# Optimization experiments

Hardware: AMD Instinct MI355X
Metric: run time of the kernel (lower is better)

The kernel has to match this reference:

```python
import jax, jax.numpy as jnp
import numpy as np

B, S, D, H = 2, 2048, 1024, 16
DK = D // H


def setup_inputs() -> dict:
    key = jax.random.key(0)
    ks = jax.random.split(key, 11)
    std = 1.0 / np.sqrt(D)
    inp = {
        "query": jax.random.normal(ks[0], (B, S, D), jnp.float32),
        "key": jax.random.normal(ks[1], (B, S, D), jnp.float32),
        "value": jax.random.normal(ks[2], (B, S, D), jnp.float32),
        # True = masked position (torch masked_fill semantics); causal mask
        "mask": jnp.triu(jnp.ones((1, 1, S, S), jnp.bool_), k=1),
        "Wq": jax.random.normal(ks[3], (D, D), jnp.float32) * std,
        "bq": jnp.zeros((D,), jnp.float32),
        "Wk": jax.random.normal(ks[4], (D, D), jnp.float32) * std,
        "bk": jnp.zeros((D,), jnp.float32),
        "Wv": jax.random.normal(ks[5], (D, D), jnp.float32) * std,
        "bv": jnp.zeros((D,), jnp.float32),
        "Wo": jax.random.normal(ks[6], (D, D), jnp.float32) * std,
        "bo": jnp.zeros((D,), jnp.float32),
    }
    return inp


def _split_heads(x):
    b, s, _ = x.shape
    return x.reshape(b, s, H, DK).transpose(0, 2, 1, 3)  # [b, H, s, dk]


def reference(query, key, value, mask, Wq, bq, Wk, bk, Wv, bv, Wo, bo):
    q = _split_heads(query @ Wq + bq)
    k = _split_heads(key @ Wk + bk)
    v = _split_heads(value @ Wv + bv)
    scale = 1.0 / (DK ** 0.5)
    logits = jnp.einsum("bhqd,bhkd->bhqk", q, k) * scale
    logits = jnp.where(mask, -1.0e9, logits)
    w = jax.nn.softmax(logits, axis=-1)
    att = jnp.einsum("bhqk,bhkd->bhqd", w, v)  # [B, H, S, dk]
    # NOTE: faithful to the original bug -- view() without permuting heads back,
    # i.e. a raw row-major reshape [B,H,S,dk] -> [B,S,H*dk].
    att = att.reshape(att.shape[0], att.shape[2], -1)
    out = att @ Wo + bo
    return out
```

## Files before the change

kernel.cpp:

```cpp
#include <hip/hip_runtime.h>
#include <hip/hip_bf16.h>

typedef __hip_bfloat16 bf16;
typedef __attribute__((ext_vector_type(8))) short bf16x8;
typedef __attribute__((ext_vector_type(4))) float f32x4;

constexpr int Bc  = 2;
constexpr int Sc  = 2048;
constexpr int Dc  = 1024;
constexpr int Hc  = 16;
constexpr int DKc = 64;

__device__ __forceinline__ float bfbits2f(unsigned short u) {
  return __uint_as_float(((unsigned)u) << 16);
}
__device__ __forceinline__ unsigned short f2bfbits(float x) {
  bf16 h = __float2bfloat16(x);
  return *reinterpret_cast<unsigned short*>(&h);
}
__device__ __forceinline__ void store1_dyn(char* base, size_t ei, int isf32, float v) {
  if (isf32) *reinterpret_cast<float*>(base + ei * 4) = v;
  else       *reinterpret_cast<bf16*>(base + ei * 2) = __float2bfloat16(v);
}
__device__ __forceinline__ float fast_exp2(float x) {
  return __builtin_amdgcn_exp2f(x);
}
__device__ __forceinline__ unsigned pkbf16(float a, float b) {
  __hip_bfloat162 h = __float22bfloat162_rn(make_float2(a, b));
  return *reinterpret_cast<unsigned*>(&h);
}
__device__ __forceinline__ uint4 pack8(const float4& a, const float4& b) {
  uint4 r;
  r.x = pkbf16(a.x, a.y);
  r.y = pkbf16(a.z, a.w);
  r.z = pkbf16(b.x, b.y);
  r.w = pkbf16(b.z, b.w);
  return r;
}
__device__ __forceinline__ void gld16(const void* g, void* l) {
  __builtin_amdgcn_global_load_lds(
      (const __attribute__((address_space(1))) unsigned int*)g,
      (__attribute__((address_space(3))) unsigned int*)l, 16, 0, 0);
}

__global__ void detect_dtype(const unsigned short* __restrict__ q, int* __restrict__ flag) {
  __shared__ int cnt[256];
  const int tid = threadIdx.x;
  int c = 0;
  for (int i = tid; i < 2048; i += 256) {
    const unsigned short u = q[i];
    const int e = (u >> 7) & 0xFF;
    if (e >= 134 || e <= 90) ++c;
  }
  cnt[tid] = c;
  __syncthreads();
  for (int s = 128; s > 0; s >>= 1) {
    if (tid < s) cnt[tid] += cnt[tid + s];
    __syncthreads();
  }
  if (tid == 0) flag[0] = (cnt[0] > 64) ? 1 : 0;
}

__global__ __launch_bounds__(256)
void prep_all(const char* __restrict__ W0, const char* __restrict__ W1,
              const char* __restrict__ W2, const char* __restrict__ W3,
              unsigned short* __restrict__ Wt_all,
              const char* __restrict__ b0, const char* __restrict__ b1,
              const char* __restrict__ b2, const char* __restrict__ b3,
              unsigned short* __restrict__ bb_all,
              const char* __restrict__ A0, const char* __restrict__ A1,
              const char* __restrict__ A2, bf16* __restrict__ B0,
              bf16* __restrict__ B1, bf16* __restrict__ B2,
              const int* __restrict__ flagp) {
  __shared__ unsigned short T[64][72];
  const int dyn = flagp[0];
  const int id = blockIdx.x;
  const int tid = threadIdx.x;

  if (id < 1024) {
    const int z = id >> 8, rem = id & 255;
    const int n0 = (rem & 15) * 64, k0 = (rem >> 4) * 64;
    const char* W = (z == 0) ? W0 : (z == 1) ? W1 : (z == 2) ? W2 : W3;
    unsigned short* Wt = Wt_all + (size_t)z * Dc * Dc;
    const int r = tid >> 2, c16 = (tid & 3) * 16;

    unsigned short us[16];
    if (dyn) {
      const float4* p = reinterpret_cast<const float4*>(
          W + ((size_t)(k0 + r) * Dc + n0 + c16) * 4);
      const float4 f0 = p[0], f1 = p[1], f2 = p[2], f3 = p[3];
      const float fv[16] = {f0.x, f0.y, f0.z, f0.w, f1.x, f1.y, f1.z, f1.w,
                            f2.x, f2.y, f2.z, f2.w, f3.x, f3.y, f3.z, f3.w};
#pragma unroll
      for (int i = 0; i < 16; ++i) us[i] = f2bfbits(fv[i]);
    } else {
      const ushort4* p = reinterpret_cast<const ushort4*>(
          W + ((size_t)(k0 + r) * Dc + n0 + c16) * 2);
      const ushort4 u0 = p[0], u1 = p[1], u2 = p[2], u3 = p[3];
      us[0] = u0.x;  us[1] = u0.y;  us[2] = u0.z;  us[3] = u0.w;
      us[4] = u1.x;  us[5] = u1.y;  us[6] = u1.z;  us[7] = u1.w;
      us[8] = u2.x;  us[9] = u2.y;  us[10] = u2.z; us[11] = u2.w;
      us[12] = u3.x; us[13] = u3.y; us[14] = u3.z; us[15] = u3.w;
    }
#pragma unroll
    for (int i = 0; i < 16; ++i) T[r][c16 + i] = us[i];
    __syncthreads();

    unsigned vs[8];
#pragma unroll
    for (int i = 0; i < 8; ++i)
      vs[i] = (unsigned)T[c16 + 2 * i][r] | ((unsigned)T[c16 + 2 * i + 1][r] << 16);
    uint4* op = reinterpret_cast<uint4*>(Wt + (size_t)(n0 + r) * Dc + k0 + c16);
    op[0] = make_uint4(vs[0], vs[1], vs[2], vs[3]);
    op[1] = make_uint4(vs[4], vs[5], vs[6], vs[7]);
  } else if (id < 2560) {
    const int j = id - 1024;
    const int z = j >> 9, x = j & 511;
    const char* src = (z == 0) ? A0 : (z == 1) ? A1 : A2;
    bf16* dst = (z == 0) ? B0 : (z == 1) ? B1 : B2;
    const size_t n = (size_t)4096 * Dc;
    const size_t stride = (size_t)512 * 256 * 8;
    for (size_t i = ((size_t)x * 256 + tid) * 8; i < n; i += stride) {
      uint4 u;
      if (dyn) {
        const float4* p = reinterpret_cast<const float4*>(src + i * 4);
        u = pack8(p[0], p[1]);
      } else {
        u = *reinterpret_cast<const uint4*>(src + i * 2);
      }
      *reinterpret_cast<uint4*>(dst + i) = u;
    }
  } else {
    const int x = id - 2560;
    const char* src = (x == 0) ? b0 : (x == 1) ? b1 : (x == 2) ? b2 : b3;
    for (int i = tid; i < Dc; i += 256) {
      float v = dyn ? reinterpret_cast<const float*>(src)[i]
                    : bfbits2f(reinterpret_cast<const unsigned short*>(src)[i]);
      bb_all[x * Dc + i] = f2bfbits(v);
    }
  }
}

__global__ __launch_bounds__(256)
void qkv_gemm_async(const bf16* __restrict__ A0, const bf16* __restrict__ A1,
                    const bf16* __restrict__ A2,
                    const unsigned short* __restrict__ Wt_all,
                    const unsigned short* __restrict__ bias_all,
                    bf16* __restrict__ C0, bf16* __restrict__ C1,
                    bf16* __restrict__ C2) {
  constexpr int K = Dc, N = Dc;
  __shared__ __align__(16) unsigned short At[128 * 32];
  __shared__ __align__(16) unsigned short Bt[128 * 32];

  const int z = blockIdx.z;
  const bf16* A = (z == 0) ? A0 : (z == 1) ? A1 : A2;
  bf16* C = (z == 0) ? C0 : (z == 1) ? C1 : C2;
  const float scale = (z == 0) ? 0.18033688011112042f : 1.0f;
  const unsigned short* Wt = Wt_all + (size_t)z * Dc * Dc;
  const unsigned short* bias = bias_all + z * Dc;

  const int tid = threadIdx.x;
  const int m0 = blockIdx.x * 128, n0 = blockIdx.y * 128;
  const int w = tid >> 6, lane = tid & 63;
  const int lo16 = lane & 15, quad = lane >> 4;
  const int wm = (w >> 1) * 64, wn = (w & 1) * 64;

  unsigned short* ldsA = &At[w * 1024 + lane * 8];
  unsigned short* ldsB = &Bt[w * 1024 + lane * 8];
  const bf16* gA = A + (size_t)(m0 + w * 32 + (lane >> 2)) * K + (lane & 3) * 8;
  const unsigned short* gB = Wt + (size_t)(n0 + w * 32 + (lane >> 2)) * K + (lane & 3) * 8;

  f32x4 acc[4][4] = {};

  for (int k0 = 0; k0 < K; k0 += 32) {
    gld16(gA + k0, ldsA);
    gld16(gA + (size_t)16 * K + k0, ldsA + 512);
    gld16(gB + k0, ldsB);
    gld16(gB + (size_t)16 * K + k0, ldsB + 512);
    __syncthreads();

    bf16x8 afr[4], bfr[4];
#pragma unroll
    for (int mt = 0; mt < 4; ++mt)
      afr[mt] = *reinterpret_cast<const bf16x8*>(&At[(wm + mt * 16 + lo16) * 32 + quad * 8]);
#pragma unroll
    for (int nt = 0; nt < 4; ++nt)
      bfr[nt] = *reinterpret_cast<const bf16x8*>(&Bt[(wn + nt * 16 + lo16) * 32 + quad * 8]);
#pragma unroll
    for (int mt = 0; mt < 4; ++mt)
#pragma unroll
      for (int nt = 0; nt < 4; ++nt)
        acc[mt][nt] = __builtin_amdgcn_mfma_f32_16x16x32_bf16(afr[mt], bfr[nt],
                                                              acc[mt][nt], 0, 0, 0);
    __syncthreads();
  }

  float bv[4];
#pragma unroll
  for (int nt = 0; nt < 4; ++nt)
    bv[nt] = bfbits2f(bias[n0 + wn + nt * 16 + lo16]);
#pragma unroll
  for (int mt = 0; mt < 4; ++mt)
#pragma unroll
    for (int r = 0; r < 4; ++r) {
      const int row = m0 + wm + mt * 16 + quad * 4 + r;
#pragma unroll
      for (int nt = 0; nt < 4; ++nt) {
        const int col = n0 + wn + nt * 16 + lo16;
        C[(size_t)row * N + col] = __float2bfloat16((acc[mt][nt][r] + bv[nt]) * scale);
      }
    }
}

__global__ __launch_bounds__(256)
void qkv_gemm(const char* __restrict__ A0, const char* __restrict__ A1,
              const char* __restrict__ A2, const unsigned short* __restrict__ Wt_all,
              const unsigned short* __restrict__ bias_all,
              bf16* __restrict__ C0, bf16* __restrict__ C1, bf16* __restrict__ C2,
              const int* __restrict__ flagp) {
  constexpr int K = Dc, N = Dc;
  __shared__ __align__(16) unsigned short At[128][32];
  __shared__ __align__(16) unsigned short Bt[128][32];

  const int z = blockIdx.z;
  const char* A = (z == 0) ? A0 : (z == 1) ? A1 : A2;
  bf16* C = (z == 0) ? C0 : (z == 1) ? C1 : C2;
  const float scale = (z == 0) ? 0.18033688011112042f : 1.0f;
  const unsigned short* Wt = Wt_all + (size_t)z * Dc * Dc;
  const unsigned short* bias = bias_all + z * Dc;
  const int af = flagp[0];

  const int tid = threadIdx.x;
  const int m0 = blockIdx.x * 128, n0 = blockIdx.y * 128;
  const int w = tid >> 6, lane = tid & 63;
  const int lo16 = lane & 15, quad = lane >> 4;
  const int wm = (w >> 1) * 64, wn = (w & 1) * 64;
  const int sr = tid >> 1, sh = (tid & 1) * 16;

  f32x4 acc[4][4] = {};

  for (int k0 = 0; k0 < K; k0 += 32) {
    uint4 a_lo, a_hi;
    if (af) {
      const float4* p = reinterpret_cast<const float4*>(
          A + ((size_t)(m0 + sr) * K + k0 + sh) * 4);
      a_lo = pack8(p[0], p[1]);
      a_hi = pack8(p[2], p[3]);
    } else {
      const uint4* p = reinterpret_cast<const uint4*>(
          A + ((size_t)(m0 + sr) * K + k0 + sh) * 2);
      a_lo = p[0];
      a_hi = p[1];
    }
    const uint4* wp = reinterpret_cast<const uint4*>(Wt + (size_t)(n0 + sr) * K + k0 + sh);
    const uint4 b_lo = wp[0], b_hi = wp[1];

    __syncthreads();
    *reinterpret_cast<uint4*>(&At[sr][sh])     = a_lo;
    *reinterpret_cast<uint4*>(&At[sr][sh + 8]) = a_hi;
    *reinterpret_cast<uint4*>(&Bt[sr][sh])     = b_lo;
    *reinterpret_cast<uint4*>(&Bt[sr][sh + 8]) = b_hi;
    __syncthreads();

    bf16x8 afr[4], bfr[4];
#pragma unroll
    for (int mt = 0; mt < 4; ++mt)
      afr[mt] = *reinterpret_cast<const bf16x8*>(&At[wm + mt * 16 + lo16][quad * 8]);
#pragma unroll
    for (int nt = 0; nt < 4; ++nt)
      bfr[nt] = *reinterpret_cast<const bf16x8*>(&Bt[wn + nt * 16 + lo16][quad * 8]);
#pragma unroll
    for (int mt = 0; mt < 4; ++mt)
#pragma unroll
      for (int nt = 0; nt < 4; ++nt)
        acc[mt][nt] = __builtin_amdgcn_mfma_f32_16x16x32_bf16(afr[mt], bfr[nt],
                                                              acc[mt][nt], 0, 0, 0);
  }

  float bv[4];
#pragma unroll
  for (int nt = 0; nt < 4; ++nt)
    bv[nt] = bfbits2f(bias[n0 + wn + nt * 16 + lo16]);
#pragma unroll
  for (int mt = 0; mt < 4; ++mt)
#pragma unroll
    for (int r = 0; r < 4; ++r) {
      const int row = m0 + wm + mt * 16 + quad * 4 + r;
#pragma unroll
      for (int nt = 0; nt < 4; ++nt) {
        const int col = n0 + wn + nt * 16 + lo16;
        C[(size_t)row * N + col] = __float2bfloat16((acc[mt][nt][r] + bv[nt]) * scale);
      }
    }
}

__global__ __launch_bounds__(256)
void out_gemm_async(const bf16* __restrict__ A, const unsigned short* __restrict__ Wt,
                    const unsigned short* __restrict__ bias, char* __restrict__ C,
                    const int* __restrict__ flagp) {
  constexpr int K = Dc, N = Dc;
  __shared__ __align__(16) unsigned short At[64 * 32];
  __shared__ __align__(16) unsigned short Bt[128 * 32];

  const int cf = flagp[0];
  const int tid = threadIdx.x;
  const int m0 = blockIdx.x * 64, n0 = blockIdx.y * 128;
  const int w = tid >> 6, lane = tid & 63;
  const int lo16 = lane & 15, quad = lane >> 4;
  const int wm = (w >> 1) * 32, wn = (w & 1) * 64;

  unsigned short* ldsA = &At[w * 512 + lane * 8];
  unsigned short* ldsB = &Bt[w * 1024 + lane * 8];
  const bf16* gA = A + (size_t)(m0 + w * 16 + (lane >> 2)) * K + (lane & 3) * 8;
  const unsigned short* gB = Wt + (size_t)(n0 + w * 32 + (lane >> 2)) * K + (lane & 3) * 8;

  f32x4 acc[2][4] = {};

  for (int k0 = 0; k0 < K; k0 += 32) {
    gld16(gA + k0, ldsA);
    gld16(gB + k0, ldsB);
    gld16(gB + (size_t)16 * K + k0, ldsB + 512);
    __syncthreads();

    bf16x8 afr[2], bfr[4];
#pragma unroll
    for (int mt = 0; mt < 2; ++mt)
      afr[mt] = *reinterpret_cast<const bf16x8*>(&At[(wm + mt * 16 + lo16) * 32 + quad * 8]);
#pragma unroll
    for (int nt = 0; nt < 4; ++nt)
      bfr[nt] = *reinterpret_cast<const bf16x8*>(&Bt[(wn + nt * 16 + lo16) * 32 + quad * 8]);
#pragma unroll
    for (int mt = 0; mt < 2; ++mt)
#pragma unroll
      for (int nt = 0; nt < 4; ++nt)
        acc[mt][nt] = __builtin_amdgcn_mfma_f32_16x16x32_bf16(afr[mt], bfr[nt],
                                                              acc[mt][nt], 0, 0, 0);
    __syncthreads();
  }

  float bv[4];
#pragma unroll
  for (int nt = 0; nt < 4; ++nt)
    bv[nt] = bfbits2f(bias[n0 + wn + nt * 16 + lo16]);
#pragma unroll
  for (int mt = 0; mt < 2; ++mt)
#pragma unroll
    for (int r = 0; r < 4; ++r) {
      const int row = m0 + wm + mt * 16 + quad * 4 + r;
#pragma unroll
      for (int nt = 0; nt < 4; ++nt) {
        const int col = n0 + wn + nt * 16 + lo16;
        store1_dyn(C, (size_t)row * N + col, cf, acc[mt][nt][r] + bv[nt]);
      }
    }
}

__global__ __launch_bounds__(512)
void attn_mfma(const bf16* __restrict__ Q, const bf16* __restrict__ K,
               const bf16* __restrict__ V, bf16* __restrict__ O) {
  __shared__ __align__(16) unsigned short Kt[64][72];
  __shared__ __align__(16) unsigned short Vt[64][72];
  __shared__ __align__(16) unsigned short St[8][16][72];
  __shared__ float Li[8][16];

  const int hb = blockIdx.x & 31;
  const int i  = blockIdx.x >> 5;
  const int g = i >> 3, r0 = i & 7;
  const int c = g ? (15 - r0) : r0;
  const int b = hb >> 4, h = hb & 15;
  const int q0 = c * 128;
  const int tid = threadIdx.x;
  const int w = tid >> 6;
  const int lane = tid & 63;
  const int lo16 = lane & 15, quad = lane >> 4;
  const size_t hd = (size_t)h * DKc;

  const int t256 = tid & 255;
  const int kr = t256 >> 2, kc = (t256 & 3) * 16;
  const int vk = (t256 & 31) * 2, vd0 = (t256 >> 5) * 8;
  const bool vrole = (w < 4);

  const bf16* qrow = Q + ((size_t)(b * Sc + q0 + w * 16 + lo16)) * Dc + hd;
  const bf16x8 qa0 = *reinterpret_cast<const bf16x8*>(qrow + quad * 8);
  const bf16x8 qa1 = *reinterpret_cast<const bf16x8*>(qrow + 32 + quad * 8);

  f32x4 oacc[4] = {f32x4{0,0,0,0}, f32x4{0,0,0,0}, f32x4{0,0,0,0}, f32x4{0,0,0,0}};
  float lsum = 0.f;
  const int qg  = q0 + w * 16 + lo16;
  const int qwm = q0 + w * 16 + 15;
  const int nt = 2 * (c + 1);

  const bf16* vsrc = V + ((size_t)(b * Sc + vk)) * Dc + hd + vd0;
  const bf16* ksrc = K + ((size_t)(b * Sc + kr)) * Dc + hd + kc;

  uint4 rA, rB;
  if (vrole) {
    rA = *reinterpret_cast<const uint4*>(vsrc);
    rB = *reinterpret_cast<const uint4*>(vsrc + Dc);
  } else {
    rA = *reinterpret_cast<const uint4*>(ksrc);
    rB = *reinterpret_cast<const uint4*>(ksrc + 8);
  }

  for (int t = 0; t < nt; ++t) {
    const int kt = t * 64;
    __syncthreads();
    if (vrole) {
      *reinterpret_cast<unsigned*>(&Vt[vd0 + 0][vk]) = (rA.x & 0xffffu) | (rB.x << 16);
      *reinterpret_cast<unsigned*>(&Vt[vd0 + 1][vk]) = (rA.x >> 16)     | (rB.x & 0xffff0000u);
      *reinterpret_cast<unsigned*>(&Vt[vd0 + 2][vk]) = (rA.y & 0xffffu) | (rB.y << 16);
      *reinterpret_cast<unsigned*>(&Vt[vd0 + 3][vk]) = (rA.y >> 16)     | (rB.y & 0xffff0000u);
      *reinterpret_cast<unsigned*>(&Vt[vd0 + 4][vk]) = (rA.z & 0xffffu) | (rB.z << 16);
      *reinterpret_cast<unsigned*>(&Vt[vd0 + 5][vk]) = (rA.z >> 16)     | (rB.z & 0xffff0000u);
      *reinterpret_cast<unsigned*>(&Vt[vd0 + 6][vk]) = (rA.w & 0xffffu) | (rB.w << 16);
      *reinterpret_cast<unsigned*>(&Vt[vd0 + 7][vk]) = (rA.w >> 16)     | (rB.w & 0xffff0000u);
    } else {
      *reinterpret_cast<uint4*>(&Kt[kr][kc])     = rA;
      *reinterpret_cast<uint4*>(&Kt[kr][kc + 8]) = rB;
    }
    __syncthreads();

    if (t + 1 < nt) {
      const size_t off = (size_t)(kt + 64) * Dc;
      if (vrole) {
        rA = *reinterpret_cast<const uint4*>(vsrc + off);
        rB = *reinterpret_cast<const uint4*>(vsrc + off + Dc);
      } else {
        rA = *reinterpret_cast<const uint4*>(ksrc + off);
        rB = *reinterpret_cast<const uint4*>(ksrc + off + 8);
      }
    }

    if (kt > qwm) continue;

    f32x4 s[4] = {f32x4{0,0,0,0}, f32x4{0,0,0,0}, f32x4{0,0,0,0}, f32x4{0,0,0,0}};
    __builtin_amdgcn_s_setprio(1);
#pragma unroll
    for (int ct = 0; ct < 4; ++ct) {
      const bf16x8 ka0 = *reinterpret_cast<const bf16x8*>(&Kt[ct * 16 + lo16][quad * 8]);
      const bf16x8 ka1 = *reinterpret_cast<const bf16x8*>(&Kt[ct * 16 + lo16][32 + quad * 8]);
      s[ct] = __builtin_amdgcn_mfma_f32_16x16x32_bf16(ka0, qa0, s[ct], 0, 0, 0);
      s[ct] = __builtin_amdgcn_mfma_f32_16x16x32_bf16(ka1, qa1, s[ct], 0, 0, 0);
    }
    __builtin_amdgcn_s_setprio(0);

    if (kt + 63 > q0 + w * 16) {
#pragma unroll
      for (int ct = 0; ct < 4; ++ct)
#pragma unroll
        for (int r = 0; r < 4; ++r)
          if (kt + ct * 16 + quad * 4 + r > qg) s[ct][r] = -1e9f;
    }

#pragma unroll
    for (int ct = 0; ct < 4; ++ct) {
      const float p0 = fast_exp2(s[ct][0]);
      const float p1 = fast_exp2(s[ct][1]);
      const float p2 = fast_exp2(s[ct][2]);
      const float p3 = fast_exp2(s[ct][3]);
      lsum += (p0 + p1) + (p2 + p3);
      uint2 pk;
      pk.x = pkbf16(p0, p1);
      pk.y = pkbf16(p2, p3);
      *reinterpret_cast<uint2*>(&St[w][lo16][ct * 16 + quad * 4]) = pk;
    }

    const bf16x8 pa0 = *reinterpret_cast<const bf16x8*>(&St[w][lo16][quad * 8]);
    const bf16x8 pa1 = *reinterpret_cast<const bf16x8*>(&St[w][lo16][32 + quad * 8]);
    __builtin_amdgcn_s_setprio(1);
#pragma unroll
    for (int ct = 0; ct < 4; ++ct) {
      const bf16x8 vb0 = *reinterpret_cast<const bf16x8*>(&Vt[ct * 16 + lo16][quad * 8]);
      const bf16x8 vb1 = *reinterpret_cast<const bf16x8*>(&Vt[ct * 16 + lo16][32 + quad * 8]);
      oacc[ct] = __builtin_amdgcn_mfma_f32_16x16x32_bf16(pa0, vb0, oacc[ct], 0, 0, 0);
      oacc[ct] = __builtin_amdgcn_mfma_f32_16x16x32_bf16(pa1, vb1, oacc[ct], 0, 0, 0);
    }
    __builtin_amdgcn_s_setprio(0);
  }

  lsum += __shfl_xor(lsum, 16);
  lsum += __shfl_xor(lsum, 32);
  if (quad == 0) Li[w][lo16] = 1.f / lsum;
  __builtin_amdgcn_wave_barrier();
  const f32x4 invv = *reinterpret_cast<const f32x4*>(&Li[w][quad * 4]);

#pragma unroll
  for (int r = 0; r < 4; ++r) {
    bf16* op = O + (((size_t)(b * Hc + h) * Sc) + q0 + w * 16 + quad * 4 + r) * DKc + lo16;
#pragma unroll
    for (int ct = 0; ct < 4; ++ct)
      op[ct * 16] = __float2bfloat16(oacc[ct][r] * invv[r]);
  }
}

extern "C" void kernel_launch(void* const* d_in, const int* in_sizes, int n_in,
                              void* d_out, int out_size, void* d_ws, size_t ws_size,
                              hipStream_t stream) {
  (void)in_sizes; (void)out_size;
  const char* query = (const char*)d_in[0];
  const char* key_  = (const char*)d_in[1];
  const char* value = (const char*)d_in[2];
  const int wb = n_in - 8;
  const char* Wq = (const char*)d_in[wb + 0];
  const char* bq = (const char*)d_in[wb + 1];
  const char* Wk = (const char*)d_in[wb + 2];
  const char* bk = (const char*)d_in[wb + 3];
  const char* Wv = (const char*)d_in[wb + 4];
  const char* bv = (const char*)d_in[wb + 5];
  const char* Wo = (const char*)d_in[wb + 6];
  const char* bo = (const char*)d_in[wb + 7];

  char* ws = (char*)d_ws;
  bf16* Qs  = (bf16*)(ws);
  bf16* Ks  = (bf16*)(ws + ((size_t)8  << 20));
  bf16* Vs  = (bf16*)(ws + ((size_t)16 << 20));
  bf16* att = (bf16*)(ws + ((size_t)24 << 20));
  unsigned short* Wt_all = (unsigned short*)(ws + ((size_t)32 << 20));
  unsigned short* bb_all = (unsigned short*)(ws + ((size_t)40 << 20));
  int* flag = (int*)(ws + ((size_t)40 << 20) + 16384);
  bf16* Qb = (bf16*)(ws + ((size_t)42 << 20));
  bf16* Kb = (bf16*)(ws + ((size_t)50 << 20));
  bf16* Vb = (bf16*)(ws + ((size_t)58 << 20));
  const bool big_ws = ws_size >= ((size_t)66 << 20);

  detect_dtype<<<1, 256, 0, stream>>>((const unsigned short*)query, flag);

  if (big_ws) {
    prep_all<<<2564, 256, 0, stream>>>(Wq, Wk, Wv, Wo, Wt_all, bq, bk, bv, bo,
                                       bb_all, query, key_, value, Qb, Kb, Vb, flag);
    qkv_gemm_async<<<dim3(32, 8, 3), 256, 0, stream>>>(Qb, Kb, Vb, Wt_all, bb_all,
                                                       Qs, Ks, Vs);
  } else {
    prep_all<<<1028, 256, 0, stream>>>(Wq, Wk, Wv, Wo, Wt_all, bq, bk, bv, bo,
                                       bb_all, query, key_, value,
                                       (bf16*)att, (bf16*)att, (bf16*)att, flag);
    qkv_gemm<<<dim3(32, 8, 3), 256, 0, stream>>>(query, key_, value, Wt_all, bb_all,
                                                 Qs, Ks, Vs, flag);
  }

  attn_mfma<<<dim3(512), 512, 0, stream>>>(Qs, Ks, Vs, att);

  out_gemm_async<<<dim3(64, 8), 256, 0, stream>>>(att, Wt_all + (size_t)3 * Dc * Dc,
                                                  bb_all + 3 * Dc, (char*)d_out, flag);
}
```

Measured before the change: 239.7 us.

## Load K fragments directly from global and double-buffer V tile with single barrier

The attention kernel stops staging K in shared memory. Each wave loads its K MFMA operands straight from global/L2 into registers. V staging is spread across all 512 threads with half-width loads, and the V tile is double-buffered so each iteration needs one barrier instead of two. Launch bounds now request higher occupancy. The trade-off is that each wave issues redundant global K reads (8 waves each read the full K tile) and pays more global latency on the critical path before the QK MFMAs.

```diff
diff --git a/kernel.cpp b/kernel.cpp
--- a/kernel.cpp
+++ b/kernel.cpp
@@ -355,11 +355,10 @@
     }
 }
 
-__global__ __launch_bounds__(512)
+__global__ __launch_bounds__(512, 4)
 void attn_mfma(const bf16* __restrict__ Q, const bf16* __restrict__ K,
                const bf16* __restrict__ V, bf16* __restrict__ O) {
-  __shared__ __align__(16) unsigned short Kt[64][72];
-  __shared__ __align__(16) unsigned short Vt[64][72];
+  __shared__ __align__(16) unsigned short Vt[2][64][72];
   __shared__ __align__(16) unsigned short St[8][16][72];
   __shared__ float Li[8][16];
 
@@ -375,10 +374,7 @@
   const int lo16 = lane & 15, quad = lane >> 4;
   const size_t hd = (size_t)h * DKc;
 
-  const int t256 = tid & 255;
-  const int kr = t256 >> 2, kc = (t256 & 3) * 16;
-  const int vk = (t256 & 31) * 2, vd0 = (t256 >> 5) * 8;
-  const bool vrole = (w < 4);
+  const int vk = (tid & 31) * 2, vd0 = (tid >> 5) * 4;
 
   const bf16* qrow = Q + ((size_t)(b * Sc + q0 + w * 16 + lo16)) * Dc + hd;
   const bf16x8 qa0 = *reinterpret_cast<const bf16x8*>(qrow + quad * 8);
@@ -390,92 +386,83 @@
   const int qwm = q0 + w * 16 + 15;
   const int nt = 2 * (c + 1);
 
-  const bf16* vsrc = V + ((size_t)(b * Sc + vk)) * Dc + hd + vd0;
-  const bf16* ksrc = K + ((size_t)(b * Sc + kr)) * Dc + hd + kc;
-
-  uint4 rA, rB;
-  if (vrole) {
-    rA = *reinterpret_cast<const uint4*>(vsrc);
-    rB = *reinterpret_cast<const uint4*>(vsrc + Dc);
-  } else {
-    rA = *reinterpret_cast<const uint4*>(ksrc);
-    rB = *reinterpret_cast<const uint4*>(ksrc + 8);
-  }
+  const bf16* vsrc  = V + ((size_t)(b * Sc + vk)) * Dc + hd + vd0;
+  const bf16* kfrag = K + ((size_t)(b * Sc) + lo16) * Dc + hd + quad * 8;
+
+  uint2 rA = *reinterpret_cast<const uint2*>(vsrc);
+  uint2 rB = *reinterpret_cast<const uint2*>(vsrc + Dc);
 
   for (int t = 0; t < nt; ++t) {
     const int kt = t * 64;
-    __syncthreads();
-    if (vrole) {
-      *reinterpret_cast<unsigned*>(&Vt[vd0 + 0][vk]) = (rA.x & 0xffffu) | (rB.x << 16);
-      *reinterpret_cast<unsigned*>(&Vt[vd0 + 1][vk]) = (rA.x >> 16)     | (rB.x & 0xffff0000u);
-      *reinterpret_cast<unsigned*>(&Vt[vd0 + 2][vk]) = (rA.y & 0xffffu) | (rB.y << 16);
-      *reinterpret_cast<unsigned*>(&Vt[vd0 + 3][vk]) = (rA.y >> 16)     | (rB.y & 0xffff0000u);
-      *reinterpret_cast<unsigned*>(&Vt[vd0 + 4][vk]) = (rA.z & 0xffffu) | (rB.z << 16);
-      *reinterpret_cast<unsigned*>(&Vt[vd0 + 5][vk]) = (rA.z >> 16)     | (rB.z & 0xffff0000u);
-      *reinterpret_cast<unsigned*>(&Vt[vd0 + 6][vk]) = (rA.w & 0xffffu) | (rB.w << 16);
-      *reinterpret_cast<unsigned*>(&Vt[vd0 + 7][vk]) = (rA.w >> 16)     | (rB.w & 0xffff0000u);
-    } else {
-      *reinterpret_cast<uint4*>(&Kt[kr][kc])     = rA;
-      *reinterpret_cast<uint4*>(&Kt[kr][kc + 8]) = rB;
-    }
-    __syncthreads();
+    const int p = t & 1;
+
+    *reinterpret_cast<unsigned*>(&Vt[p][vd0 + 0][vk]) = (rA.x & 0xffffu) | (rB.x << 16);
+    *reinterpret_cast<unsigned*>(&Vt[p][vd0 + 1][vk]) = (rA.x >> 16)     | (rB.x & 0xffff0000u);
+    *reinterpret_cast<unsigned*>(&Vt[p][vd0 + 2][vk]) = (rA.y & 0xffffu) | (rB.y << 16);
+    *reinterpret_cast<unsigned*>(&Vt[p][vd0 + 3][vk]) = (rA.y >> 16)     | (rB.y & 0xffff0000u);
+    __syncthreads();
+
+    const bool live = (kt <= qwm);
+
+    bf16x8 ka[4], kb[4];
+    if (live) {
+      const bf16* kp = kfrag + (size_t)kt * Dc;
+#pragma unroll
+      for (int ct = 0; ct < 4; ++ct) {
+        ka[ct] = *reinterpret_cast<const bf16x8*>(kp + (size_t)(ct * 16) * Dc);
+        kb[ct] = *reinterpret_cast<const bf16x8*>(kp + (size_t)(ct * 16) * Dc + 32);
+      }
+    }
 
     if (t + 1 < nt) {
-      const size_t off = (size_t)(kt + 64) * Dc;
-      if (vrole) {
-        rA = *reinterpret_cast<const uint4*>(vsrc + off);
-        rB = *reinterpret_cast<const uint4*>(vsrc + off + Dc);
-      } else {
-        rA = *reinterpret_cast<const uint4*>(ksrc + off);
-        rB = *reinterpret_cast<const uint4*>(ksrc + off + 8);
-      }
-    }
-
-    if (kt > qwm) continue;
-
-    f32x4 s[4] = {f32x4{0,0,0,0}, f32x4{0,0,0,0}, f32x4{0,0,0,0}, f32x4{0,0,0,0}};
-    __builtin_amdgcn_s_setprio(1);
-#pragma unroll
-    for (int ct = 0; ct < 4; ++ct) {
-      const bf16x8 ka0 = *reinterpret_cast<const bf16x8*>(&Kt[ct * 16 + lo16][quad * 8]);
-      const bf16x8 ka1 = *reinterpret_cast<const bf16x8*>(&Kt[ct * 16 + lo16][32 + quad * 8]);
-      s[ct] = __builtin_amdgcn_mfma_f32_16x16x32_bf16(ka0, qa0, s[ct], 0, 0, 0);
-      s[ct] = __builtin_amdgcn_mfma_f32_16x16x32_bf16(ka1, qa1, s[ct], 0, 0, 0);
-    }
-    __builtin_amdgcn_s_setprio(0);
-
-    if (kt + 63 > q0 + w * 16) {
-#pragma unroll
-      for (int ct = 0; ct < 4; ++ct)
-#pragma unroll
-        for (int r = 0; r < 4; ++r)
-          if (kt + ct * 16 + quad * 4 + r > qg) s[ct][r] = -1e9f;
-    }
-
-#pragma unroll
-    for (int ct = 0; ct < 4; ++ct) {
-      const float p0 = fast_exp2(s[ct][0]);
-      const float p1 = fast_exp2(s[ct][1]);
-      const float p2 = fast_exp2(s[ct][2]);
-      const float p3 = fast_exp2(s[ct][3]);
-      lsum += (p0 + p1) + (p2 + p3);
-      uint2 pk;
-      pk.x = pkbf16(p0, p1);
-      pk.y = pkbf16(p2, p3);
-      *reinterpret_cast<uint2*>(&St[w][lo16][ct * 16 + quad * 4]) = pk;
-    }
-
-    const bf16x8 pa0 = *reinterpret_cast<const bf16x8*>(&St[w][lo16][quad * 8]);
-    const bf16x8 pa1 = *reinterpret_cast<const bf16x8*>(&St[w][lo16][32 + quad * 8]);
-    __builtin_amdgcn_s_setprio(1);
-#pragma unroll
-    for (int ct = 0; ct < 4; ++ct) {
-      const bf16x8 vb0 = *reinterpret_cast<const bf16x8*>(&Vt[ct * 16 + lo16][quad * 8]);
-      const bf16x8 vb1 = *reinterpret_cast<const bf16x8*>(&Vt[ct * 16 + lo16][32 + quad * 8]);
-      oacc[ct] = __builtin_amdgcn_mfma_f32_16x16x32_bf16(pa0, vb0, oacc[ct], 0, 0, 0);
-      oacc[ct] = __builtin_amdgcn_mfma_f32_16x16x32_bf16(pa1, vb1, oacc[ct], 0, 0, 0);
-    }
-    __builtin_amdgcn_s_setprio(0);
+      const size_t off = (size_t)(t + 1) * 64 * Dc;
+      rA = *reinterpret_cast<const uint2*>(vsrc + off);
+      rB = *reinterpret_cast<const uint2*>(vsrc + off + Dc);
+    }
+
+    if (live) {
+      f32x4 s[4] = {f32x4{0,0,0,0}, f32x4{0,0,0,0}, f32x4{0,0,0,0}, f32x4{0,0,0,0}};
+      __builtin_amdgcn_s_setprio(1);
+#pragma unroll
+      for (int ct = 0; ct < 4; ++ct) {
+        s[ct] = __builtin_amdgcn_mfma_f32_16x16x32_bf16(ka[ct], qa0, s[ct], 0, 0, 0);
+        s[ct] = __builtin_amdgcn_mfma_f32_16x16x32_bf16(kb[ct], qa1, s[ct], 0, 0, 0);
+      }
+      __builtin_amdgcn_s_setprio(0);
+
+      if (kt + 63 > q0 + w * 16) {
+#pragma unroll
+        for (int ct = 0; ct < 4; ++ct)
+#pragma unroll
+          for (int r = 0; r < 4; ++r)
+            if (kt + ct * 16 + quad * 4 + r > qg) s[ct][r] = -1e9f;
+      }
+
+#pragma unroll
+      for (int ct = 0; ct < 4; ++ct) {
+        const float p0 = fast_exp2(s[ct][0]);
+        const float p1 = fast_exp2(s[ct][1]);
+        const float p2 = fast_exp2(s[ct][2]);
+        const float p3 = fast_exp2(s[ct][3]);
+        lsum += (p0 + p1) + (p2 + p3);
+        uint2 pk;
+        pk.x = pkbf16(p0, p1);
+        pk.y = pkbf16(p2, p3);
+        *reinterpret_cast<uint2*>(&St[w][lo16][ct * 16 + quad * 4]) = pk;
+      }
+
+      const bf16x8 pa0 = *reinterpret_cast<const bf16x8*>(&St[w][lo16][quad * 8]);
+      const bf16x8 pa1 = *reinterpret_cast<const bf16x8*>(&St[w][lo16][32 + quad * 8]);
+      __builtin_amdgcn_s_setprio(1);
+#pragma unroll
+      for (int ct = 0; ct < 4; ++ct) {
+        const bf16x8 vb0 = *reinterpret_cast<const bf16x8*>(&Vt[p][ct * 16 + lo16][quad * 8]);
+        const bf16x8 vb1 = *reinterpret_cast<const bf16x8*>(&Vt[p][ct * 16 + lo16][32 + quad * 8]);
+        oacc[ct] = __builtin_amdgcn_mfma_f32_16x16x32_bf16(pa0, vb0, oacc[ct], 0, 0, 0);
+        oacc[ct] = __builtin_amdgcn_mfma_f32_16x16x32_bf16(pa1, vb1, oacc[ct], 0, 0, 0);
+      }
+      __builtin_amdgcn_s_setprio(0);
+    }
   }
 
   lsum += __shfl_xor(lsum, 16);
```

Measured after the change: 282.9 us. +18.0%, slower.
